# Kernel optimization log

Measured on AMD Instinct MI355X. Metric: run time of the kernel, lower is better.

The kernel has to match this reference:

```python
import jax, jax.numpy as jnp
import numpy as np

N = 100000
E = 1600000
DIMS = [256, 192, 128, 64, 3]  # in_features=256, hidden_layer_count=4, last layer -> 3


def setup_inputs() -> dict:
    key = jax.random.key(0)
    ks = jax.random.split(key, 2 + 4 * len(DIMS))
    features = jax.random.normal(ks[0], (N, 256), dtype=jnp.float32)
    # (torch.unique-based normalization implicitly assumes this)
    src = jnp.arange(E, dtype=jnp.int64) % N
    dst = jax.random.randint(ks[1], (E,), 0, N, dtype=jnp.int64)
    edges = jnp.stack([src, dst], axis=1)
    inp = {"features": features, "edges": edges}
    ki = 2
    for li in range(4):
        din, dout = DIMS[li], DIMS[li + 1]
        s = 1.0 / np.sqrt(din)
        inp[f"W0_{li}"] = jax.random.uniform(ks[ki], (din, dout), jnp.float32, -s, s); ki += 1
        inp[f"b0_{li}"] = jax.random.uniform(ks[ki], (dout,), jnp.float32, -s, s); ki += 1
        inp[f"W1_{li}"] = jax.random.uniform(ks[ki], (din, dout), jnp.float32, -s, s); ki += 1
        inp[f"b1_{li}"] = jax.random.uniform(ks[ki], (dout,), jnp.float32, -s, s); ki += 1
    return inp


def _graph_conv_norm(x, edges, deg_inv, W0, b0, W1, b1):
    # pytorch3d GraphConv (undirected): w0(x) + scatter-add of w1(x[neighbor]) over both edge directions,
    # then degree normalization (GraphConvNorm)
    h0 = x @ W0 + b0                       # [N, dout]
    h1 = x @ W1 + b1                       # [N, dout]
    agg = jnp.zeros_like(h0)
    agg = agg.at[edges[:, 0]].add(h1[edges[:, 1]])
    agg = agg.at[edges[:, 1]].add(h1[edges[:, 0]])
    return deg_inv * (h0 + agg)


def reference(features, edges, W0_0, b0_0, W1_0, b1_0, W0_1, b0_1, W1_1, b1_1,
              W0_2, b0_2, W1_2, b1_2, W0_3, b0_3, W1_3, b1_3):
    # degree = occurrence count of each vertex id in edges (== torch.unique(..., return_counts=True)[1])
    deg = jnp.zeros((N,), jnp.float32).at[edges.reshape(-1)].add(1.0)
    deg_inv = (1.0 / deg)[:, None]
    params = [(W0_0, b0_0, W1_0, b1_0), (W0_1, b0_1, W1_1, b1_1), (W0_2, b0_2, W1_2, b1_2)]
    x = features
    for (W0, b0, W1, b1) in params:
        x = jax.nn.relu(_graph_conv_norm(x, edges, deg_inv, W0, b0, W1, b1))
    return _graph_conv_norm(x, edges, deg_inv, W0_3, b0_3, W1_3, b1_3)
```

## Files before the change

### kernel.cpp

```cpp
#include <hip/hip_runtime.h>
#include <hip/hip_fp16.h>

#define NV 100000
#define NE 1600000

#define BM 64
#define BN 64
#define BK 16

#define SCAN_B 1024
#define NBLK ((NV + SCAN_B - 1) / SCAN_B)

typedef __attribute__((ext_vector_type(8))) _Float16 f16x8;
typedef __attribute__((ext_vector_type(4))) _Float16 f16x4;
typedef __attribute__((ext_vector_type(2))) _Float16 f16x2;
typedef __attribute__((ext_vector_type(4))) float f32x4;

__global__ void degree_count(const int* __restrict__ ef, int* __restrict__ deg, int n) {
    int i = blockIdx.x * blockDim.x + threadIdx.x;
    if (i < n) atomicAdd(&deg[ef[i]], 1);
}

__global__ __launch_bounds__(SCAN_B) void scan_block(const int* __restrict__ deg,
                                                     int* __restrict__ part,
                                                     int* __restrict__ bsum, int n) {
    __shared__ int tmp[SCAN_B];
    const int tid = threadIdx.x;
    const int gid = blockIdx.x * SCAN_B + tid;
    int v = (gid < n) ? deg[gid] : 0;
    tmp[tid] = v;
    __syncthreads();
    for (int off = 1; off < SCAN_B; off <<= 1) {
        int t = (tid >= off) ? tmp[tid - off] : 0;
        __syncthreads();
        tmp[tid] += t;
        __syncthreads();
    }
    if (gid < n) part[gid] = tmp[tid] - v;
    if (tid == SCAN_B - 1) bsum[blockIdx.x] = tmp[tid];
}

__global__ __launch_bounds__(128) void scan_top(int* __restrict__ bsum, int nb) {
    __shared__ int tmp[128];
    const int tid = threadIdx.x;
    int v = (tid < nb) ? bsum[tid] : 0;
    tmp[tid] = v;
    __syncthreads();
    for (int off = 1; off < 128; off <<= 1) {
        int t = (tid >= off) ? tmp[tid - off] : 0;
        __syncthreads();
        tmp[tid] += t;
        __syncthreads();
    }
    if (tid < nb) bsum[tid] = tmp[tid] - v;
}

__global__ __launch_bounds__(SCAN_B) void finalize_rowptr(int* __restrict__ rowptr,
                                                          const int* __restrict__ bsum,
                                                          const int* __restrict__ deg,
                                                          int* __restrict__ fill,
                                                          float* __restrict__ dinv, int n) {
    const int gid = blockIdx.x * SCAN_B + threadIdx.x;
    if (gid < n) {
        int r = rowptr[gid] + bsum[blockIdx.x];
        rowptr[gid] = r;
        fill[gid] = r;
        dinv[gid] = 1.0f / (float)deg[gid];
    }
    if (gid == 0) rowptr[n] = 2 * NE;
}

__global__ void fill_adj(const int* __restrict__ edges, int* __restrict__ fill,
                         int* __restrict__ adj, int nE) {
    int e = blockIdx.x * blockDim.x + threadIdx.x;
    if (e >= nE) return;
    const int a = edges[2 * e];
    const int b = edges[2 * e + 1];
    int pa = atomicAdd(&fill[a], 1); adj[pa] = b;
    int pb = atomicAdd(&fill[b], 1); adj[pb] = a;
}

template <typename XT, int DIN, int NT>
__global__ __launch_bounds__(256) void gemm_dual_panel(
    const XT* __restrict__ X,
    const float* __restrict__ W0, const float* __restrict__ b0,
    const float* __restrict__ W1, const float* __restrict__ b1,
    _Float16* __restrict__ C0, _Float16* __restrict__ C1, int M)
{
    constexpr int DOUT = NT * 64;
    constexpr int AST = DIN + 12;
    constexpr int BST = 44;

    __shared__ _Float16 As[96 * AST];
    __shared__ _Float16 Bs[2][64 * BST];

    const int tid = threadIdx.x;
    const int bm = blockIdx.x * 96;
    const int lane = tid & 63;
    const int wid = tid >> 6;
    const int wm = wid >> 1;
    const int wn = wid & 1;
    const int lr = lane & 15;
    const int lk = lane >> 4;

    if constexpr (sizeof(XT) == 4) {
        constexpr int QPR = DIN / 4;
        for (int idx = tid; idx < 96 * QPR; idx += 256) {
            const int row = idx / QPR, q = idx % QPR;
            const int grow = bm + row;
            float4 v = {0.f, 0.f, 0.f, 0.f};
            if (grow < M)
                v = *reinterpret_cast<const float4*>(&X[(size_t)grow * DIN + q * 4]);
            f16x4 h = { (_Float16)v.x, (_Float16)v.y, (_Float16)v.z, (_Float16)v.w };
            *reinterpret_cast<f16x4*>(&As[row * AST + q * 4]) = h;
        }
    } else {
        constexpr int QPR = DIN / 8;
        for (int idx = tid; idx < 96 * QPR; idx += 256) {
            const int row = idx / QPR, q = idx % QPR;
            const int grow = bm + row;
            f16x8 h = {};
            if (grow < M)
                h = *reinterpret_cast<const f16x8*>(&X[(size_t)grow * DIN + q * 8]);
            *reinterpret_cast<f16x8*>(&As[row * AST + q * 8]) = h;
        }
    }
    __syncthreads();

    const int ccol = tid & 63;
    const int kb = (tid >> 6) * 8;

    #pragma unroll
    for (int nt = 0; nt < NT; ++nt) {
        const int bn = nt * 64;
        f32x4 acc[2][3][2] = {};

        for (int k0 = 0; k0 < DIN; k0 += 32) {
            {
                const float* pw0 = &W0[(size_t)(k0 + kb) * DOUT + bn + ccol];
                const float* pw1 = &W1[(size_t)(k0 + kb) * DOUT + bn + ccol];
                _Float16* d0 = &Bs[0][ccol * BST + kb];
                _Float16* d1 = &Bs[1][ccol * BST + kb];
                #pragma unroll
                for (int i = 0; i < 8; ++i) {
                    d0[i] = (_Float16)pw0[(size_t)i * DOUT];
                    d1[i] = (_Float16)pw1[(size_t)i * DOUT];
                }
            }
            __syncthreads();

            f16x8 a[3], b[2][2];
            #pragma unroll
            for (int mf = 0; mf < 3; ++mf)
                a[mf] = *reinterpret_cast<const f16x8*>(
                    &As[(wm * 48 + mf * 16 + lr) * AST + k0 + lk * 8]);
            #pragma unroll
            for (int o = 0; o < 2; ++o)
                #pragma unroll
                for (int nf = 0; nf < 2; ++nf)
                    b[o][nf] = *reinterpret_cast<const f16x8*>(
                        &Bs[o][(wn * 32 + nf * 16 + lr) * BST + lk * 8]);

            #pragma unroll
            for (int o = 0; o < 2; ++o)
                #pragma unroll
                for (int mf = 0; mf < 3; ++mf)
                    #pragma unroll
                    for (int nf = 0; nf < 2; ++nf)
                        acc[o][mf][nf] = __builtin_amdgcn_mfma_f32_16x16x32_f16(
                            a[mf], b[o][nf], acc[o][mf][nf], 0, 0, 0);

            __syncthreads();
        }

        #pragma unroll
        for (int mf = 0; mf < 3; ++mf) {
            #pragma unroll
            for (int reg = 0; reg < 4; ++reg) {
                const int row = bm + wm * 48 + mf * 16 + lk * 4 + reg;
                if (row >= M) continue;
                #pragma unroll
                for (int nf = 0; nf < 2; ++nf) {
                    const int c = bn + wn * 32 + nf * 16 + lr;
                    C0[(size_t)row * DOUT + c] = (_Float16)(acc[0][mf][nf][reg] + b0[c]);
                    C1[(size_t)row * DOUT + c] = (_Float16)(acc[1][mf][nf][reg] + b1[c]);
                }
            }
        }
    }
}

__global__ __launch_bounds__(256) void gemm_dual_bias_f32(
    const _Float16* __restrict__ X,
    const float* __restrict__ W0, const float* __restrict__ b0,
    const float* __restrict__ W1, const float* __restrict__ b1,
    float* __restrict__ C0, float* __restrict__ C1,
    int M, int din, int dout)
{
    __shared__ float As[BM][BK + 1];
    __shared__ float Bs0[BK][BN];
    __shared__ float Bs1[BK][BN];

    const int tid = threadIdx.x;
    const int bm = blockIdx.x * BM;
    const int bn = blockIdx.y * BN;
    const int tx = tid & 15;
    const int ty = tid >> 4;

    const int ar = tid >> 2;
    const int ac = (tid & 3) * 4;
    const int br = tid >> 4;
    const int bc = (tid & 15) * 4;

    float acc0[4][4] = {};
    float acc1[4][4] = {};

    for (int k0 = 0; k0 < din; k0 += BK) {
        {
            const int grow = bm + ar;
            if (grow < M) {
                const f16x4 v = *reinterpret_cast<const f16x4*>(&X[(size_t)grow * din + k0 + ac]);
                As[ar][ac + 0] = (float)v[0]; As[ar][ac + 1] = (float)v[1];
                As[ar][ac + 2] = (float)v[2]; As[ar][ac + 3] = (float)v[3];
            } else {
                As[ar][ac + 0] = 0.f; As[ar][ac + 1] = 0.f;
                As[ar][ac + 2] = 0.f; As[ar][ac + 3] = 0.f;
            }
        }
        {
            const int gk = k0 + br;
            const int gc = bn + bc;
            float4 v0, v1;
            v0.x = (gc + 0 < dout) ? W0[(size_t)gk * dout + gc + 0] : 0.f;
            v0.y = (gc + 1 < dout) ? W0[(size_t)gk * dout + gc + 1] : 0.f;
            v0.z = (gc + 2 < dout) ? W0[(size_t)gk * dout + gc + 2] : 0.f;
            v0.w = (gc + 3 < dout) ? W0[(size_t)gk * dout + gc + 3] : 0.f;
            v1.x = (gc + 0 < dout) ? W1[(size_t)gk * dout + gc + 0] : 0.f;
            v1.y = (gc + 1 < dout) ? W1[(size_t)gk * dout + gc + 1] : 0.f;
            v1.z = (gc + 2 < dout) ? W1[(size_t)gk * dout + gc + 2] : 0.f;
            v1.w = (gc + 3 < dout) ? W1[(size_t)gk * dout + gc + 3] : 0.f;
            *reinterpret_cast<float4*>(&Bs0[br][bc]) = v0;
            *reinterpret_cast<float4*>(&Bs1[br][bc]) = v1;
        }
        __syncthreads();

        #pragma unroll
        for (int kk = 0; kk < BK; ++kk) {
            const float a0 = As[ty * 4 + 0][kk];
            const float a1 = As[ty * 4 + 1][kk];
            const float a2 = As[ty * 4 + 2][kk];
            const float a3 = As[ty * 4 + 3][kk];
            const float4 p = *reinterpret_cast<const float4*>(&Bs0[kk][tx * 4]);
            const float4 q = *reinterpret_cast<const float4*>(&Bs1[kk][tx * 4]);
            acc0[0][0] += a0 * p.x; acc0[0][1] += a0 * p.y; acc0[0][2] += a0 * p.z; acc0[0][3] += a0 * p.w;
            acc0[1][0] += a1 * p.x; acc0[1][1] += a1 * p.y; acc0[1][2] += a1 * p.z; acc0[1][3] += a1 * p.w;
            acc0[2][0] += a2 * p.x; acc0[2][1] += a2 * p.y; acc0[2][2] += a2 * p.z; acc0[2][3] += a2 * p.w;
            acc0[3][0] += a3 * p.x; acc0[3][1] += a3 * p.y; acc0[3][2] += a3 * p.z; acc0[3][3] += a3 * p.w;
            acc1[0][0] += a0 * q.x; acc1[0][1] += a0 * q.y; acc1[0][2] += a0 * q.z; acc1[0][3] += a0 * q.w;
            acc1[1][0] += a1 * q.x; acc1[1][1] += a1 * q.y; acc1[1][2] += a1 * q.z; acc1[1][3] += a1 * q.w;
            acc1[2][0] += a2 * q.x; acc1[2][1] += a2 * q.y; acc1[2][2] += a2 * q.z; acc1[2][3] += a2 * q.w;
            acc1[3][0] += a3 * q.x; acc1[3][1] += a3 * q.y; acc1[3][2] += a3 * q.z; acc1[3][3] += a3 * q.w;
        }
        __syncthreads();
    }

    #pragma unroll
    for (int i = 0; i < 4; ++i) {
        const int row = bm + ty * 4 + i;
        if (row >= M) continue;
        #pragma unroll
        for (int j = 0; j < 4; ++j) {
            const int col = bn + tx * 4 + j;
            if (col < dout) {
                C0[(size_t)row * dout + col] = acc0[i][j] + b0[col];
                C1[(size_t)row * dout + col] = acc1[i][j] + b1[col];
            }
        }
    }
}

__global__ __launch_bounds__(256) void gather_d192_h(
    const _Float16* __restrict__ h0, const __half2* __restrict__ h1,
    const int* __restrict__ rowptr, const int* __restrict__ adj,
    const float* __restrict__ dinv, _Float16* __restrict__ out)
{
    const int v = blockIdx.x * 4 + (threadIdx.x >> 6);
    if (v >= NV) return;
    const int lane = threadIdx.x & 63;
    const int sub = lane >> 5;
    const int cu = (lane & 31) * 3;
    const int s = rowptr[v], e = rowptr[v + 1];

    float2 a0 = {0.f, 0.f}, a1 = {0.f, 0.f}, a2 = {0.f, 0.f};

    int j = s;
    const int jend = s + ((e - s) & ~7);
    for (; j < jend; j += 8) {
        const int u0 = adj[j + 0 + sub];
        const int u1 = adj[j + 2 + sub];
        const int u2 = adj[j + 4 + sub];
        const int u3 = adj[j + 6 + sub];
        const __half2* r0 = h1 + (size_t)u0 * 96 + cu;
        const __half2* r1 = h1 + (size_t)u1 * 96 + cu;
        const __half2* r2 = h1 + (size_t)u2 * 96 + cu;
        const __half2* r3 = h1 + (size_t)u3 * 96 + cu;
        const __half2 x00 = r0[0], x01 = r0[1], x02 = r0[2];
        const __half2 x10 = r1[0], x11 = r1[1], x12 = r1[2];
        const __half2 x20 = r2[0], x21 = r2[1], x22 = r2[2];
        const __half2 x30 = r3[0], x31 = r3[1], x32 = r3[2];
        float2 p;
        p = __half22float2(x00); a0.x += p.x; a0.y += p.y;
        p = __half22float2(x01); a1.x += p.x; a1.y += p.y;
        p = __half22float2(x02); a2.x += p.x; a2.y += p.y;
        p = __half22float2(x10); a0.x += p.x; a0.y += p.y;
        p = __half22float2(x11); a1.x += p.x; a1.y += p.y;
        p = __half22float2(x12); a2.x += p.x; a2.y += p.y;
        p = __half22float2(x20); a0.x += p.x; a0.y += p.y;
        p = __half22float2(x21); a1.x += p.x; a1.y += p.y;
        p = __half22float2(x22); a2.x += p.x; a2.y += p.y;
        p = __half22float2(x30); a0.x += p.x; a0.y += p.y;
        p = __half22float2(x31); a1.x += p.x; a1.y += p.y;
        p = __half22float2(x32); a2.x += p.x; a2.y += p.y;
    }
    for (; j < e; j += 2) {
        const int jj = j + sub;
        if (jj < e) {
            const __half2* r = h1 + (size_t)adj[jj] * 96 + cu;
            float2 p;
            p = __half22float2(r[0]); a0.x += p.x; a0.y += p.y;
            p = __half22float2(r[1]); a1.x += p.x; a1.y += p.y;
            p = __half22float2(r[2]); a2.x += p.x; a2.y += p.y;
        }
    }

    a0.x += __shfl_xor(a0.x, 32); a0.y += __shfl_xor(a0.y, 32);
    a1.x += __shfl_xor(a1.x, 32); a1.y += __shfl_xor(a1.y, 32);
    a2.x += __shfl_xor(a2.x, 32); a2.y += __shfl_xor(a2.y, 32);

    if (sub == 0) {
        const float di = dinv[v];
        const size_t base = (size_t)v * 192 + (size_t)cu * 2;
        const f16x2 z0 = *reinterpret_cast<const f16x2*>(h0 + base + 0);
        const f16x2 z1 = *reinterpret_cast<const f16x2*>(h0 + base + 2);
        const f16x2 z2 = *reinterpret_cast<const f16x2*>(h0 + base + 4);
        f16x2 o0, o1, o2;
        o0[0] = (_Float16)fmaxf(((float)z0[0] + a0.x) * di, 0.f);
        o0[1] = (_Float16)fmaxf(((float)z0[1] + a0.y) * di, 0.f);
        o1[0] = (_Float16)fmaxf(((float)z1[0] + a1.x) * di, 0.f);
        o1[1] = (_Float16)fmaxf(((float)z1[1] + a1.y) * di, 0.f);
        o2[0] = (_Float16)fmaxf(((float)z2[0] + a2.x) * di, 0.f);
        o2[1] = (_Float16)fmaxf(((float)z2[1] + a2.y) * di, 0.f);
        *reinterpret_cast<f16x2*>(out + base + 0) = o0;
        *reinterpret_cast<f16x2*>(out + base + 2) = o1;
        *reinterpret_cast<f16x2*>(out + base + 4) = o2;
    }
}

__global__ __launch_bounds__(256) void gather_d128_h(
    const _Float16* __restrict__ h0, const __half2* __restrict__ h1,
    const int* __restrict__ rowptr, const int* __restrict__ adj,
    const float* __restrict__ dinv, _Float16* __restrict__ out)
{
    const int v = blockIdx.x * 4 + (threadIdx.x >> 6);
    if (v >= NV) return;
    const int lane = threadIdx.x & 63;
    const int sub = lane >> 4;
    const int cu = (lane & 15) * 4;
    const int s = rowptr[v], e = rowptr[v + 1];

    float acc[8] = {};

    int j = s;
    const int jend = s + ((e - s) & ~15);
    for (; j < jend; j += 16) {
        const int u0 = adj[j + 0 + sub];
        const int u1 = adj[j + 4 + sub];
        const int u2 = adj[j + 8 + sub];
        const int u3 = adj[j + 12 + sub];
        const int4 w0 = *reinterpret_cast<const int4*>(h1 + (size_t)u0 * 64 + cu);
        const int4 w1 = *reinterpret_cast<const int4*>(h1 + (size_t)u1 * 64 + cu);
        const int4 w2 = *reinterpret_cast<const int4*>(h1 + (size_t)u2 * 64 + cu);
        const int4 w3 = *reinterpret_cast<const int4*>(h1 + (size_t)u3 * 64 + cu);
        #pragma unroll
        for (int t = 0; t < 4; ++t) {
            const float2 p0 = __half22float2(*(const __half2*)(&(&w0.x)[t]));
            const float2 p1 = __half22float2(*(const __half2*)(&(&w1.x)[t]));
            const float2 p2 = __half22float2(*(const __half2*)(&(&w2.x)[t]));
            const float2 p3 = __half22float2(*(const __half2*)(&(&w3.x)[t]));
            acc[2 * t + 0] += (p0.x + p1.x) + (p2.x + p3.x);
            acc[2 * t + 1] += (p0.y + p1.y) + (p2.y + p3.y);
        }
    }
    for (; j < e; j += 4) {
        const int jj = j + sub;
        if (jj < e) {
            const int4 w0 = *reinterpret_cast<const int4*>(h1 + (size_t)adj[jj] * 64 + cu);
            #pragma unroll
            for (int t = 0; t < 4; ++t) {
                const float2 p = __half22float2(*(const __half2*)(&(&w0.x)[t]));
                acc[2 * t + 0] += p.x;
                acc[2 * t + 1] += p.y;
            }
        }
    }

    #pragma unroll
    for (int t = 0; t < 8; ++t) {
        acc[t] += __shfl_xor(acc[t], 16);
        acc[t] += __shfl_xor(acc[t], 32);
    }

    if (sub == 0) {
        const float di = dinv[v];
        const size_t base = (size_t)v * 128 + (size_t)cu * 2;
        const f16x8 z = *reinterpret_cast<const f16x8*>(h0 + base);
        f16x8 o;
        #pragma unroll
        for (int t = 0; t < 8; ++t)
            o[t] = (_Float16)fmaxf(((float)z[t] + acc[t]) * di, 0.f);
        *reinterpret_cast<f16x8*>(out + base) = o;
    }
}

__global__ __launch_bounds__(256) void gather_d64_h(
    const _Float16* __restrict__ h0, const __half2* __restrict__ h1,
    const int* __restrict__ rowptr, const int* __restrict__ adj,
    const float* __restrict__ dinv, _Float16* __restrict__ out)
{
    const int v = blockIdx.x * 4 + (threadIdx.x >> 6);
    if (v >= NV) return;
    const int lane = threadIdx.x & 63;
    const int sub = lane >> 4;
    const int cu = (lane & 15) * 2;
    const int s = rowptr[v], e = rowptr[v + 1];

    float acc[4] = {};

    int j = s;
    const int jend = s + ((e - s) & ~15);
    for (; j < jend; j += 16) {
        const int u0 = adj[j + 0 + sub];
        const int u1 = adj[j + 4 + sub];
        const int u2 = adj[j + 8 + sub];
        const int u3 = adj[j + 12 + sub];
        const int2 w0 = *reinterpret_cast<const int2*>(h1 + (size_t)u0 * 32 + cu);
        const int2 w1 = *reinterpret_cast<const int2*>(h1 + (size_t)u1 * 32 + cu);
        const int2 w2 = *reinterpret_cast<const int2*>(h1 + (size_t)u2 * 32 + cu);
        const int2 w3 = *reinterpret_cast<const int2*>(h1 + (size_t)u3 * 32 + cu);
        #pragma unroll
        for (int t = 0; t < 2; ++t) {
            const float2 p0 = __half22float2(*(const __half2*)(&(&w0.x)[t]));
            const float2 p1 = __half22float2(*(const __half2*)(&(&w1.x)[t]));
            const float2 p2 = __half22float2(*(const __half2*)(&(&w2.x)[t]));
            const float2 p3 = __half22float2(*(const __half2*)(&(&w3.x)[t]));
            acc[2 * t + 0] += (p0.x + p1.x) + (p2.x + p3.x);
            acc[2 * t + 1] += (p0.y + p1.y) + (p2.y + p3.y);
        }
    }
    for (; j < e; j += 4) {
        const int jj = j + sub;
        if (jj < e) {
            const int2 w0 = *reinterpret_cast<const int2*>(h1 + (size_t)adj[jj] * 32 + cu);
            #pragma unroll
            for (int t = 0; t < 2; ++t) {
                const float2 p = __half22float2(*(const __half2*)(&(&w0.x)[t]));
                acc[2 * t + 0] += p.x;
                acc[2 * t + 1] += p.y;
            }
        }
    }

    #pragma unroll
    for (int t = 0; t < 4; ++t) {
        acc[t] += __shfl_xor(acc[t], 16);
        acc[t] += __shfl_xor(acc[t], 32);
    }

    if (sub == 0) {
        const float di = dinv[v];
        const size_t base = (size_t)v * 64 + (size_t)cu * 2;
        const f16x4 z = *reinterpret_cast<const f16x4*>(h0 + base);
        f16x4 o;
        #pragma unroll
        for (int t = 0; t < 4; ++t)
            o[t] = (_Float16)fmaxf(((float)z[t] + acc[t]) * di, 0.f);
        *reinterpret_cast<f16x4*>(out + base) = o;
    }
}

__global__ __launch_bounds__(256) void gather_d3(
    const float* __restrict__ h0, const float* __restrict__ h1,
    const int* __restrict__ rowptr, const int* __restrict__ adj,
    const float* __restrict__ dinv, float* __restrict__ out)
{
    const int v = blockIdx.x * 4 + (threadIdx.x >> 6);
    if (v >= NV) return;
    const int lane = threadIdx.x & 63;
    const int s = rowptr[v], e = rowptr[v + 1];
    float a0 = 0.f, a1 = 0.f, a2 = 0.f;
    for (int j = s + lane; j < e; j += 64) {
        const float3 r = *reinterpret_cast<const float3*>(h1 + (size_t)adj[j] * 3);
        a0 += r.x; a1 += r.y; a2 += r.z;
    }
    #pragma unroll
    for (int off = 1; off < 64; off <<= 1) {
        a0 += __shfl_xor(a0, off);
        a1 += __shfl_xor(a1, off);
        a2 += __shfl_xor(a2, off);
    }
    if (lane == 0) {
        const float di = dinv[v];
        const size_t base = (size_t)v * 3;
        out[base + 0] = (h0[base + 0] + a0) * di;
        out[base + 1] = (h0[base + 1] + a1) * di;
        out[base + 2] = (h0[base + 2] + a2) * di;
    }
}

extern "C" void kernel_launch(void* const* d_in, const int* in_sizes, int n_in,
                              void* d_out, int out_size, void* d_ws, size_t ws_size,
                              hipStream_t stream) {
    const float* features = (const float*)d_in[0];
    const int*   edges    = (const int*)d_in[1];

    char* ws = (char*)d_ws;
    size_t off = 0;
    auto alloc = [&](size_t bytes) {
        void* p = ws + off;
        off = (off + bytes + 255) & ~(size_t)255;
        return p;
    };
    int*      deg    = (int*)alloc((size_t)NV * sizeof(int));
    float*    dinv   = (float*)alloc((size_t)NV * sizeof(float));
    int*      rowptr = (int*)alloc((size_t)(NV + 1) * sizeof(int));
    int*      fill   = (int*)alloc((size_t)NV * sizeof(int));
    int*      bsum   = (int*)alloc(256 * sizeof(int));
    int*      adj    = (int*)alloc((size_t)2 * NE * sizeof(int));
    _Float16* hC0    = (_Float16*)alloc((size_t)NV * 192 * sizeof(_Float16));
    _Float16* hC1    = (_Float16*)alloc((size_t)NV * 192 * sizeof(_Float16));
    _Float16* bufX1  = (_Float16*)alloc((size_t)NV * 192 * sizeof(_Float16));
    _Float16* bufX2  = (_Float16*)alloc((size_t)NV * 128 * sizeof(_Float16));
    float*    c0f    = (float*)alloc((size_t)NV * 3 * sizeof(float));
    float*    c1f    = (float*)alloc((size_t)NV * 3 * sizeof(float));

    hipMemsetAsync(deg, 0, (size_t)NV * sizeof(int), stream);
    degree_count<<<(2 * NE + 255) / 256, 256, 0, stream>>>(edges, deg, 2 * NE);
    scan_block<<<NBLK, SCAN_B, 0, stream>>>(deg, rowptr, bsum, NV);
    scan_top<<<1, 128, 0, stream>>>(bsum, NBLK);
    finalize_rowptr<<<NBLK, SCAN_B, 0, stream>>>(rowptr, bsum, deg, fill, dinv, NV);
    fill_adj<<<(NE + 255) / 256, 256, 0, stream>>>(edges, fill, adj, NE);

    const int gatherGrid = (NV + 3) / 4;
    const int panelGrid = (NV + 95) / 96;

    gemm_dual_panel<float, 256, 3><<<panelGrid, 256, 0, stream>>>(
        features,
        (const float*)d_in[2], (const float*)d_in[3],
        (const float*)d_in[4], (const float*)d_in[5],
        hC0, hC1, NV);
    gather_d192_h<<<gatherGrid, 256, 0, stream>>>(hC0, (const __half2*)hC1,
                                                  rowptr, adj, dinv, bufX1);

    gemm_dual_panel<_Float16, 192, 2><<<panelGrid, 256, 0, stream>>>(
        bufX1,
        (const float*)d_in[6], (const float*)d_in[7],
        (const float*)d_in[8], (const float*)d_in[9],
        hC0, hC1, NV);
    gather_d128_h<<<gatherGrid, 256, 0, stream>>>(hC0, (const __half2*)hC1,
                                                  rowptr, adj, dinv, bufX2);

    gemm_dual_panel<_Float16, 128, 1><<<panelGrid, 256, 0, stream>>>(
        bufX2,
        (const float*)d_in[10], (const float*)d_in[11],
        (const float*)d_in[12], (const float*)d_in[13],
        hC0, hC1, NV);
    gather_d64_h<<<gatherGrid, 256, 0, stream>>>(hC0, (const __half2*)hC1,
                                                 rowptr, adj, dinv, bufX1);

    {
        dim3 grid((NV + BM - 1) / BM, 1);
        gemm_dual_bias_f32<<<grid, 256, 0, stream>>>(
            bufX1,
            (const float*)d_in[14], (const float*)d_in[15],
            (const float*)d_in[16], (const float*)d_in[17],
            c0f, c1f, NV, 64, 3);
        gather_d3<<<gatherGrid, 256, 0, stream>>>(c0f, c1f, rowptr, adj, dinv, (float*)d_out);
    }
}
```

Measured before the change: 761.3 us.

## Hold GEMM A-operand in registers and pre-transpose weights to fp16

Weights are converted once per call into transposed fp16 copies by a small kernel, so the GEMM can load B tiles with vectorized 16-byte reads instead of strided scalar fp32 loads and per-element conversion. The A panel is no longer staged in LDS. Each wave loads its rows straight into registers for the whole K dimension, and the row tile shrinks from 96 to 64. This cuts LDS traffic and frees shared memory, which may raise occupancy, at the cost of more registers per thread (up to 16 f16x8 for DIN=256), six extra small launches, and a larger grid.

New measurement: 736.2 us. -3.3%, faster.

```diff
diff --git a/kernel.cpp b/kernel.cpp
--- a/kernel.cpp
+++ b/kernel.cpp
@@ -80,22 +80,30 @@
     int pb = atomicAdd(&fill[b], 1); adj[pb] = a;
 }
 
+__global__ void convert_wt(const float* __restrict__ W, _Float16* __restrict__ WT,
+                           int din, int dout) {
+    int i = blockIdx.x * blockDim.x + threadIdx.x;
+    if (i >= din * dout) return;
+    const int k = i / dout, n = i % dout;
+    WT[(size_t)n * din + k] = (_Float16)W[i];
+}
+
 template <typename XT, int DIN, int NT>
-__global__ __launch_bounds__(256) void gemm_dual_panel(
+__global__ __launch_bounds__(256) void gemm_dual_reg(
     const XT* __restrict__ X,
-    const float* __restrict__ W0, const float* __restrict__ b0,
-    const float* __restrict__ W1, const float* __restrict__ b1,
+    const _Float16* __restrict__ WT0, const float* __restrict__ b0,
+    const _Float16* __restrict__ WT1, const float* __restrict__ b1,
     _Float16* __restrict__ C0, _Float16* __restrict__ C1, int M)
 {
     constexpr int DOUT = NT * 64;
-    constexpr int AST = DIN + 12;
-    constexpr int BST = 44;
-
-    __shared__ _Float16 As[96 * AST];
+    constexpr int NKS = DIN / 32;
+    constexpr int NKC = DIN / 64;
+    constexpr int BST = 72;
+
     __shared__ _Float16 Bs[2][64 * BST];
 
     const int tid = threadIdx.x;
-    const int bm = blockIdx.x * 96;
+    const int bm = blockIdx.x * 64;
     const int lane = tid & 63;
     const int wid = tid >> 6;
     const int wm = wid >> 1;
@@ -103,85 +111,82 @@
     const int lr = lane & 15;
     const int lk = lane >> 4;
 
-    if constexpr (sizeof(XT) == 4) {
-        constexpr int QPR = DIN / 4;
-        for (int idx = tid; idx < 96 * QPR; idx += 256) {
-            const int row = idx / QPR, q = idx % QPR;
-            const int grow = bm + row;
-            float4 v = {0.f, 0.f, 0.f, 0.f};
-            if (grow < M)
-                v = *reinterpret_cast<const float4*>(&X[(size_t)grow * DIN + q * 4]);
-            f16x4 h = { (_Float16)v.x, (_Float16)v.y, (_Float16)v.z, (_Float16)v.w };
-            *reinterpret_cast<f16x4*>(&As[row * AST + q * 4]) = h;
-        }
-    } else {
-        constexpr int QPR = DIN / 8;
-        for (int idx = tid; idx < 96 * QPR; idx += 256) {
-            const int row = idx / QPR, q = idx % QPR;
-            const int grow = bm + row;
+    f16x8 areg[NKS][2];
+    #pragma unroll
+    for (int ks = 0; ks < NKS; ++ks) {
+        #pragma unroll
+        for (int mf = 0; mf < 2; ++mf) {
+            const int row = bm + wm * 32 + mf * 16 + lr;
+            const int k = ks * 32 + lk * 8;
             f16x8 h = {};
-            if (grow < M)
-                h = *reinterpret_cast<const f16x8*>(&X[(size_t)grow * DIN + q * 8]);
-            *reinterpret_cast<f16x8*>(&As[row * AST + q * 8]) = h;
-        }
-    }
-    __syncthreads();
-
-    const int ccol = tid & 63;
-    const int kb = (tid >> 6) * 8;
-
-    #pragma unroll
+            if (row < M) {
+                if constexpr (sizeof(XT) == 4) {
+                    const float4 v0 = *reinterpret_cast<const float4*>(&X[(size_t)row * DIN + k]);
+                    const float4 v1 = *reinterpret_cast<const float4*>(&X[(size_t)row * DIN + k + 4]);
+                    h[0] = (_Float16)v0.x; h[1] = (_Float16)v0.y;
+                    h[2] = (_Float16)v0.z; h[3] = (_Float16)v0.w;
+                    h[4] = (_Float16)v1.x; h[5] = (_Float16)v1.y;
+                    h[6] = (_Float16)v1.z; h[7] = (_Float16)v1.w;
+                } else {
+                    h = *reinterpret_cast<const f16x8*>(&X[(size_t)row * DIN + k]);
+                }
+            }
+            areg[ks][mf] = h;
+        }
+    }
+
+    const int scol = tid >> 2;
+    const int skb = (tid & 3) * 16;
+
     for (int nt = 0; nt < NT; ++nt) {
-        const int bn = nt * 64;
-        f32x4 acc[2][3][2] = {};
-
-        for (int k0 = 0; k0 < DIN; k0 += 32) {
+        f32x4 acc[2][2][2] = {};
+
+        #pragma unroll
+        for (int kc = 0; kc < NKC; ++kc) {
             {
-                const float* pw0 = &W0[(size_t)(k0 + kb) * DOUT + bn + ccol];
-                const float* pw1 = &W1[(size_t)(k0 + kb) * DOUT + bn + ccol];
-                _Float16* d0 = &Bs[0][ccol * BST + kb];
-                _Float16* d1 = &Bs[1][ccol * BST + kb];
+                const size_t srcoff = (size_t)(nt * 64 + scol) * DIN + kc * 64 + skb;
+                *reinterpret_cast<f16x8*>(&Bs[0][scol * BST + skb]) =
+                    *reinterpret_cast<const f16x8*>(&WT0[srcoff]);
+                *reinterpret_cast<f16x8*>(&Bs[0][scol * BST + skb + 8]) =
+                    *reinterpret_cast<const f16x8*>(&WT0[srcoff + 8]);
+                *reinterpret_cast<f16x8*>(&Bs[1][scol * BST + skb]) =
+                    *reinterpret_cast<const f16x8*>(&WT1[srcoff]);
+                *reinterpret_cast<f16x8*>(&Bs[1][scol * BST + skb + 8]) =
+                    *reinterpret_cast<const f16x8*>(&WT1[srcoff + 8]);
+            }
+            __syncthreads();
+
+            #pragma unroll
+            for (int k2 = 0; k2 < 2; ++k2) {
+                const int ks = kc * 2 + k2;
+                f16x8 b[2][2];
                 #pragma unroll
-                for (int i = 0; i < 8; ++i) {
-                    d0[i] = (_Float16)pw0[(size_t)i * DOUT];
-                    d1[i] = (_Float16)pw1[(size_t)i * DOUT];
-                }
-            }
-            __syncthreads();
-
-            f16x8 a[3], b[2][2];
-            #pragma unroll
-            for (int mf = 0; mf < 3; ++mf)
-                a[mf] = *reinterpret_cast<const f16x8*>(
-                    &As[(wm * 48 + mf * 16 + lr) * AST + k0 + lk * 8]);
-            #pragma unroll
-            for (int o = 0; o < 2; ++o)
-                #pragma unroll
-                for (int nf = 0; nf < 2; ++nf)
-                    b[o][nf] = *reinterpret_cast<const f16x8*>(
-                        &Bs[o][(wn * 32 + nf * 16 + lr) * BST + lk * 8]);
-
-            #pragma unroll
-            for (int o = 0; o < 2; ++o)
-                #pragma unroll
-                for (int mf = 0; mf < 3; ++mf)
+                for (int o = 0; o < 2; ++o)
                     #pragma unroll
                     for (int nf = 0; nf < 2; ++nf)
-                        acc[o][mf][nf] = __builtin_amdgcn_mfma_f32_16x16x32_f16(
-                            a[mf], b[o][nf], acc[o][mf][nf], 0, 0, 0);
-
+                        b[o][nf] = *reinterpret_cast<const f16x8*>(
+                            &Bs[o][(wn * 32 + nf * 16 + lr) * BST + k2 * 32 + lk * 8]);
+                #pragma unroll
+                for (int o = 0; o < 2; ++o)
+                    #pragma unroll
+                    for (int mf = 0; mf < 2; ++mf)
+                        #pragma unroll
+                        for (int nf = 0; nf < 2; ++nf)
+                            acc[o][mf][nf] = __builtin_amdgcn_mfma_f32_16x16x32_f16(
+                                areg[ks][mf], b[o][nf], acc[o][mf][nf], 0, 0, 0);
+            }
             __syncthreads();
         }
 
         #pragma unroll
-        for (int mf = 0; mf < 3; ++mf) {
+        for (int mf = 0; mf < 2; ++mf) {
             #pragma unroll
             for (int reg = 0; reg < 4; ++reg) {
-                const int row = bm + wm * 48 + mf * 16 + lk * 4 + reg;
+                const int row = bm + wm * 32 + mf * 16 + lk * 4 + reg;
                 if (row >= M) continue;
                 #pragma unroll
                 for (int nf = 0; nf < 2; ++nf) {
-                    const int c = bn + wn * 32 + nf * 16 + lr;
+                    const int c = nt * 64 + wn * 32 + nf * 16 + lr;
                     C0[(size_t)row * DOUT + c] = (_Float16)(acc[0][mf][nf][reg] + b0[c]);
                     C1[(size_t)row * DOUT + c] = (_Float16)(acc[1][mf][nf][reg] + b1[c]);
                 }
@@ -542,6 +547,12 @@
     _Float16* bufX2  = (_Float16*)alloc((size_t)NV * 128 * sizeof(_Float16));
     float*    c0f    = (float*)alloc((size_t)NV * 3 * sizeof(float));
     float*    c1f    = (float*)alloc((size_t)NV * 3 * sizeof(float));
+    _Float16* wt0_0  = (_Float16*)alloc((size_t)192 * 256 * sizeof(_Float16));
+    _Float16* wt1_0  = (_Float16*)alloc((size_t)192 * 256 * sizeof(_Float16));
+    _Float16* wt0_1  = (_Float16*)alloc((size_t)128 * 192 * sizeof(_Float16));
+    _Float16* wt1_1  = (_Float16*)alloc((size_t)128 * 192 * sizeof(_Float16));
+    _Float16* wt0_2  = (_Float16*)alloc((size_t)64 * 128 * sizeof(_Float16));
+    _Float16* wt1_2  = (_Float16*)alloc((size_t)64 * 128 * sizeof(_Float16));
 
     hipMemsetAsync(deg, 0, (size_t)NV * sizeof(int), stream);
     degree_count<<<(2 * NE + 255) / 256, 256, 0, stream>>>(edges, deg, 2 * NE);
@@ -550,29 +561,30 @@
     finalize_rowptr<<<NBLK, SCAN_B, 0, stream>>>(rowptr, bsum, deg, fill, dinv, NV);
     fill_adj<<<(NE + 255) / 256, 256, 0, stream>>>(edges, fill, adj, NE);
 
+    convert_wt<<<(256 * 192 + 255) / 256, 256, 0, stream>>>((const float*)d_in[2],  wt0_0, 256, 192);
+    convert_wt<<<(256 * 192 + 255) / 256, 256, 0, stream>>>((const float*)d_in[4],  wt1_0, 256, 192);
+    convert_wt<<<(192 * 128 + 255) / 256, 256, 0, stream>>>((const float*)d_in[6],  wt0_1, 192, 128);
+    convert_wt<<<(192 * 128 + 255) / 256, 256, 0, stream>>>((const float*)d_in[8],  wt1_1, 192, 128);
+    convert_wt<<<(128 * 64 + 255) / 256, 256, 0, stream>>>((const float*)d_in[10], wt0_2, 128, 64);
+    convert_wt<<<(128 * 64 + 255) / 256, 256, 0, stream>>>((const float*)d_in[12], wt1_2, 128, 64);
+
     const int gatherGrid = (NV + 3) / 4;
-    const int panelGrid = (NV + 95) / 96;
-
-    gemm_dual_panel<float, 256, 3><<<panelGrid, 256, 0, stream>>>(
-        features,
-        (const float*)d_in[2], (const float*)d_in[3],
-        (const float*)d_in[4], (const float*)d_in[5],
+    const int gemmGrid = (NV + 63) / 64;
+
+    gemm_dual_reg<float, 256, 3><<<gemmGrid, 256, 0, stream>>>(
+        features, wt0_0, (const float*)d_in[3], wt1_0, (const float*)d_in[5],
         hC0, hC1, NV);
     gather_d192_h<<<gatherGrid, 256, 0, stream>>>(hC0, (const __half2*)hC1,
                                                   rowptr, adj, dinv, bufX1);
 
-    gemm_dual_panel<_Float16, 192, 2><<<panelGrid, 256, 0, stream>>>(
-        bufX1,
-        (const float*)d_in[6], (const float*)d_in[7],
-        (const float*)d_in[8], (const float*)d_in[9],
+    gemm_dual_reg<_Float16, 192, 2><<<gemmGrid, 256, 0, stream>>>(
+        bufX1, wt0_1, (const float*)d_in[7], wt1_1, (const float*)d_in[9],
         hC0, hC1, NV);
     gather_d128_h<<<gatherGrid, 256, 0, stream>>>(hC0, (const __half2*)hC1,
                                                   rowptr, adj, dinv, bufX2);
 
-    gemm_dual_panel<_Float16, 128, 1><<<panelGrid, 256, 0, stream>>>(
-        bufX2,
-        (const float*)d_in[10], (const float*)d_in[11],
-        (const float*)d_in[12], (const float*)d_in[13],
+    gemm_dual_reg<_Float16, 128, 1><<<gemmGrid, 256, 0, stream>>>(
+        bufX2, wt0_2, (const float*)d_in[11], wt1_2, (const float*)d_in[13],
         hC0, hC1, NV);
     gather_d64_h<<<gatherGrid, 256, 0, stream>>>(hC0, (const __half2*)hC1,
                                                  rowptr, adj, dinv, bufX1);
```
